# Optimization experiments

Hardware: AMD Instinct MI355X
Metric: run time of the kernel (lower is better)

Reference implementation:

```python
import jax, jax.numpy as jnp
import numpy as np

B, S, D = 2, 2048, 1024
H = 16
DH = D // H  # 64

def setup_inputs() -> dict:
    key = jax.random.key(0)
    ks = jax.random.split(key, 7)
    sc = 1.0 / np.sqrt(DH)
    return {
        "sequences": jax.random.normal(ks[0], (B, S, D), dtype=jnp.float32),
        "Wq": jax.random.normal(ks[1], (H, DH, DH), dtype=jnp.float32) * sc,
        "bq": jax.random.normal(ks[2], (H, DH), dtype=jnp.float32) * 0.02,
        "Wk": jax.random.normal(ks[3], (H, DH, DH), dtype=jnp.float32) * sc,
        "bk": jax.random.normal(ks[4], (H, DH), dtype=jnp.float32) * 0.02,
        "Wv": jax.random.normal(ks[5], (H, DH, DH), dtype=jnp.float32) * sc,
        "bv": jax.random.normal(ks[6], (H, DH), dtype=jnp.float32) * 0.02,
    }

def reference(sequences, Wq, bq, Wk, bk, Wv, bv):
    b, s, _ = sequences.shape
    x = sequences.reshape(b, s, H, DH)  # [B,S,H,Dh]
    # torch Linear: y = x @ W^T + b; W is [out,in] => einsum contracts input dim d
    q = jnp.einsum("bshd,hed->bshe", x, Wq) + bq  # [B,S,H,Dh]
    k = jnp.einsum("bshd,hed->bshe", x, Wk) + bk
    v = jnp.einsum("bshd,hed->bshe", x, Wv) + bv
    scores = jnp.einsum("bshd,bthd->bhst", q, k) / jnp.sqrt(jnp.float32(DH))
    attn = jax.nn.softmax(scores, axis=-1)  # [B,H,S,S]
    out = jnp.einsum("bhst,bthd->bshd", attn, v)  # [B,S,H,Dh]
    return out.reshape(b, s, H * DH)
```

## Files before the change

kernel.cpp:

```cpp
#include <hip/hip_runtime.h>

typedef unsigned short u16;
typedef unsigned int   u32;
typedef __bf16 bf16x8 __attribute__((ext_vector_type(8)));
typedef float  f32x4  __attribute__((ext_vector_type(4)));
typedef float  f32x16 __attribute__((ext_vector_type(16)));
typedef u16    u16x4  __attribute__((ext_vector_type(4)));
typedef u32    u32x4  __attribute__((ext_vector_type(4)));

#define HH   16
#define DHH  64
#define SEQL 2048
#define NB   2
#define BHN  (NB * HH)
#define SCLF 0.1803368801111204f

static __device__ __forceinline__ u16 f2bf(float f) {
    return __builtin_bit_cast(u16, (__bf16)f);
}
static __device__ __forceinline__ u32 pack2(float a, float b) {
    return (u32)f2bf(a) | ((u32)f2bf(b) << 16);
}
static __device__ __forceinline__ void plswap(u32 &a, u32 &b) {
    asm volatile("v_permlane32_swap_b32 %0, %1" : "+v"(a), "+v"(b));
}

static __device__ __forceinline__ void gload_lds16(const void* g, void* l) {
    __builtin_amdgcn_global_load_lds(
        (const __attribute__((address_space(1))) unsigned int*)g,
        (__attribute__((address_space(3))) unsigned int*)l, 16, 0, 0);
}

__global__ __launch_bounds__(256) void wconv_kernel(
    const float* __restrict__ Wq, const float* __restrict__ Wk,
    const float* __restrict__ Wv, u16* __restrict__ Wb)
{
    const int m = blockIdx.y;
    const float* W = (m == 0) ? Wq : (m == 1) ? Wk : Wv;
    const float s = (m == 0) ? SCLF : 1.0f;
    const int i = (blockIdx.x * 256 + threadIdx.x) * 4;
    float4 v = *reinterpret_cast<const float4*>(W + i);
    u16x4 o = { f2bf(v.x * s), f2bf(v.y * s), f2bf(v.z * s), f2bf(v.w * s) };
    *reinterpret_cast<u16x4*>(Wb + (size_t)m * 65536 + i) = o;
}

__global__ __launch_bounds__(256) void qkv_kernel(
    const float* __restrict__ x, const u16* __restrict__ Wb,
    const float* __restrict__ bq, const float* __restrict__ bk,
    const float* __restrict__ bv,
    u16* __restrict__ Qws, u16* __restrict__ Kws, u16* __restrict__ Vtws)
{
    const int h   = blockIdx.y;
    const int r0  = blockIdx.x * 64;
    const int tid = threadIdx.x;
    const int w   = tid >> 6;
    const int l   = tid & 63;
    const int c   = l & 15;
    const int g   = l >> 4;

    __shared__ u16 qt[64 * 72];
    __shared__ u16 kt[64 * 72];
    __shared__ u16 vt[64 * 72];

    bf16x8 xa[2];
    {
        const float* xp = x + (size_t)(r0 + w * 16 + c) * 1024 + h * 64 + g * 8;
        #pragma unroll
        for (int kh = 0; kh < 2; ++kh) {
            float4 lo = *reinterpret_cast<const float4*>(xp + kh * 32);
            float4 hi = *reinterpret_cast<const float4*>(xp + kh * 32 + 4);
            bf16x8 f;
            f[0]=(__bf16)lo.x; f[1]=(__bf16)lo.y; f[2]=(__bf16)lo.z; f[3]=(__bf16)lo.w;
            f[4]=(__bf16)hi.x; f[5]=(__bf16)hi.y; f[6]=(__bf16)hi.z; f[7]=(__bf16)hi.w;
            xa[kh] = f;
        }
    }

    const int b      = r0 >> 11;
    const int s_base = r0 & (SEQL - 1);
    const int bh     = b * HH + h;

    f32x4 acc[3][4];
    #pragma unroll
    for (int m = 0; m < 3; ++m)
        #pragma unroll
        for (int ct = 0; ct < 4; ++ct) {
            acc[m][ct][0] = 0.f; acc[m][ct][1] = 0.f;
            acc[m][ct][2] = 0.f; acc[m][ct][3] = 0.f;
        }
    #pragma unroll
    for (int kh = 0; kh < 2; ++kh)
        #pragma unroll
        for (int m = 0; m < 3; ++m) {
            const u16* W = Wb + (size_t)m * 65536 + h * 4096;
            #pragma unroll
            for (int ct = 0; ct < 4; ++ct) {
                bf16x8 wf = *reinterpret_cast<const bf16x8*>(
                    W + (ct * 16 + c) * 64 + kh * 32 + g * 8);
                acc[m][ct] = __builtin_amdgcn_mfma_f32_16x16x32_bf16(xa[kh], wf, acc[m][ct], 0, 0, 0);
            }
        }

    #pragma unroll
    for (int ct = 0; ct < 4; ++ct) {
        const float bbq = bq[h * 64 + ct * 16 + c] * SCLF;
        const float bbk = bk[h * 64 + ct * 16 + c];
        const float bbv = bv[h * 64 + ct * 16 + c];
        u16x4 pv;
        #pragma unroll
        for (int r = 0; r < 4; ++r) {
            const int srow = w * 16 + g * 4 + r;
            qt[srow * 72 + ct * 16 + c] = f2bf(acc[0][ct][r] + bbq);
            kt[srow * 72 + ct * 16 + c] = f2bf(acc[1][ct][r] + bbk);
            pv[r] = f2bf(acc[2][ct][r] + bbv);
        }
        *reinterpret_cast<u16x4*>(&vt[(ct * 16 + c) * 72 + w * 16 + g * 4]) = pv;
    }
    __syncthreads();

    {
        const int d  = tid >> 2;
        const int s0 = (tid & 3) * 16;
        u16* qp = Qws + ((size_t)bh * SEQL + s_base + d) * 64 + s0;
        *reinterpret_cast<uint4*>(qp)     = *reinterpret_cast<const uint4*>(&qt[d * 72 + s0]);
        *reinterpret_cast<uint4*>(qp + 8) = *reinterpret_cast<const uint4*>(&qt[d * 72 + s0 + 8]);
        u16* kp = Kws + ((size_t)bh * SEQL + s_base + d) * 64 + s0;
        *reinterpret_cast<uint4*>(kp)     = *reinterpret_cast<const uint4*>(&kt[d * 72 + s0]);
        *reinterpret_cast<uint4*>(kp + 8) = *reinterpret_cast<const uint4*>(&kt[d * 72 + s0 + 8]);
        u16* vp = Vtws + ((size_t)bh * 64 + d) * SEQL + s_base + s0;
        *reinterpret_cast<uint4*>(vp)     = *reinterpret_cast<const uint4*>(&vt[d * 72 + s0]);
        *reinterpret_cast<uint4*>(vp + 8) = *reinterpret_cast<const uint4*>(&vt[d * 72 + s0 + 8]);
    }
}

__global__ __launch_bounds__(256, 2) void attn_kernel(
    const u16* __restrict__ Qws, const u16* __restrict__ Kws,
    const u16* __restrict__ Vtws, float* __restrict__ out)
{
    const int p     = blockIdx.x;
    const int lid   = (p & 7) * 64 + (p >> 3);
    const int qtile = lid & 15;
    const int bh    = lid >> 4;
    const int b     = bh >> 4;
    const int h     = bh & 15;

    const int tid = threadIdx.x;
    const int w   = tid >> 6;
    const int l   = tid & 63;
    const int lq  = l & 31;
    const int hi  = l >> 5;
    const int q0  = qtile * 128 + w * 32;

    __shared__ u16 k_lds[2][64 * 64];
    __shared__ u16 v_lds[2][64 * 64];

    const u16* Kb = Kws  + (size_t)bh * SEQL * 64;
    const u16* Vb = Vtws + (size_t)bh * 64 * SEQL;

    const int rs8 = l >> 3;
    const int sx  = (l & 7) ^ rs8;

    #define STAGE(bb, k0)                                                     \
    {   _Pragma("unroll")                                                     \
        for (int a = 0; a < 2; ++a) {                                         \
            const int rbase = w * 16 + a * 8;                                 \
            const int r     = rbase + rs8;                                    \
            gload_lds16(Kb + (size_t)((k0) + r) * 64 + sx * 8,                \
                        &k_lds[bb][rbase * 64]);                              \
            gload_lds16(Vb + (size_t)r * SEQL + (k0) + sx * 8,                \
                        &v_lds[bb][rbase * 64]);                              \
        }                                                                     \
    }

    bf16x8 qf[4];
    #pragma unroll
    for (int s = 0; s < 4; ++s)
        qf[s] = *reinterpret_cast<const bf16x8*>(
            Qws + ((size_t)bh * SEQL + q0 + lq) * 64 + s * 16 + hi * 8);

    f32x16 zero16;
    #pragma unroll
    for (int j = 0; j < 16; ++j) zero16[j] = 0.f;

    f32x16 acc[2];
    acc[0] = zero16; acc[1] = zero16;
    float mrow = -1e30f;
    float lrow = 0.f;

    int koff[4];
    #pragma unroll
    for (int s = 0; s < 4; ++s) koff[s] = ((s * 2 + hi) ^ (lq & 7)) * 16;

    bf16x8 vfA[2][4], vfB[2][4];
    bf16x8 pfA[4], pfB[4];

    STAGE(0, 0);
    __syncthreads();

    auto body = [&](bf16x8 (&vfC)[2][4], bf16x8 (&pfC)[4],
                    bf16x8 (&vfP)[2][4], bf16x8 (&pfP)[4],
                    int t, bool has_prev) {
        const int cur = t & 1;
        if (t + 1 < SEQL / 64) STAGE(cur ^ 1, (t + 1) * 64);

        const char* kb = reinterpret_cast<const char*>(&k_lds[cur][0]);
        bf16x8 kf0[4], kf1[4];
        #pragma unroll
        for (int s = 0; s < 4; ++s) {
            kf0[s] = *reinterpret_cast<const bf16x8*>(kb + lq * 128 + koff[s]);
            kf1[s] = *reinterpret_cast<const bf16x8*>(kb + (32 + lq) * 128 + koff[s]);
        }

        __builtin_amdgcn_s_setprio(1);
        f32x16 st0 = __builtin_amdgcn_mfma_f32_32x32x16_bf16(kf0[0], qf[0], zero16, 0, 0, 0);
        f32x16 st1 = __builtin_amdgcn_mfma_f32_32x32x16_bf16(kf1[0], qf[0], zero16, 0, 0, 0);
        #pragma unroll
        for (int s = 1; s < 4; ++s) {
            st0 = __builtin_amdgcn_mfma_f32_32x32x16_bf16(kf0[s], qf[s], st0, 0, 0, 0);
            st1 = __builtin_amdgcn_mfma_f32_32x32x16_bf16(kf1[s], qf[s], st1, 0, 0, 0);
        }
        if (has_prev) {
            #pragma unroll
            for (int s = 0; s < 4; ++s) {
                acc[0] = __builtin_amdgcn_mfma_f32_32x32x16_bf16(vfP[0][s], pfP[s], acc[0], 0, 0, 0);
                acc[1] = __builtin_amdgcn_mfma_f32_32x32x16_bf16(vfP[1][s], pfP[s], acc[1], 0, 0, 0);
            }
        }
        __builtin_amdgcn_s_setprio(0);

        const char* vb = reinterpret_cast<const char*>(&v_lds[cur][0]);
        #pragma unroll
        for (int dt = 0; dt < 2; ++dt)
            #pragma unroll
            for (int s = 0; s < 4; ++s)
                vfC[dt][s] = *reinterpret_cast<const bf16x8*>(vb + (dt * 32 + lq) * 128 + koff[s]);

        float t0 = fmaxf(fmaxf(st0[0], st0[1]),  fmaxf(st0[2], st0[3]));
        float t1 = fmaxf(fmaxf(st0[4], st0[5]),  fmaxf(st0[6], st0[7]));
        float t2 = fmaxf(fmaxf(st0[8], st0[9]),  fmaxf(st0[10], st0[11]));
        float t3 = fmaxf(fmaxf(st0[12], st0[13]), fmaxf(st0[14], st0[15]));
        float t4 = fmaxf(fmaxf(st1[0], st1[1]),  fmaxf(st1[2], st1[3]));
        float t5 = fmaxf(fmaxf(st1[4], st1[5]),  fmaxf(st1[6], st1[7]));
        float t6 = fmaxf(fmaxf(st1[8], st1[9]),  fmaxf(st1[10], st1[11]));
        float t7 = fmaxf(fmaxf(st1[12], st1[13]), fmaxf(st1[14], st1[15]));
        float mx = fmaxf(fmaxf(fmaxf(t0, t1), fmaxf(t2, t3)),
                         fmaxf(fmaxf(t4, t5), fmaxf(t6, t7)));
        mx = fmaxf(mx, __shfl_xor(mx, 32, 64));

        if (!__all(mx <= mrow + 8.f)) {
            const float mn    = fmaxf(mrow, mx);
            const float alpha = __builtin_amdgcn_exp2f(mrow - mn);
            mrow = mn;
            lrow *= alpha;
            #pragma unroll
            for (int j = 0; j < 16; ++j) { acc[0][j] *= alpha; acc[1][j] *= alpha; }
        }

        float rs0 = 0.f, rs1 = 0.f;
        u32 wd[16];
        {
            float pp[16];
            #pragma unroll
            for (int r = 0; r < 16; ++r) {
                pp[r] = __builtin_amdgcn_exp2f(st0[r] - mrow);
                if (r & 1) rs1 += pp[r]; else rs0 += pp[r];
            }
            #pragma unroll
            for (int j = 0; j < 8; ++j) wd[j] = pack2(pp[2 * j], pp[2 * j + 1]);
        }
        {
            float pp[16];
            #pragma unroll
            for (int r = 0; r < 16; ++r) {
                pp[r] = __builtin_amdgcn_exp2f(st1[r] - mrow);
                if (r & 1) rs1 += pp[r]; else rs0 += pp[r];
            }
            #pragma unroll
            for (int j = 0; j < 8; ++j) wd[8 + j] = pack2(pp[2 * j], pp[2 * j + 1]);
        }
        lrow += rs0 + rs1;

        plswap(wd[0],  wd[2]);  plswap(wd[1],  wd[3]);
        plswap(wd[4],  wd[6]);  plswap(wd[5],  wd[7]);
        plswap(wd[8],  wd[10]); plswap(wd[9],  wd[11]);
        plswap(wd[12], wd[14]); plswap(wd[13], wd[15]);

        #pragma unroll
        for (int s = 0; s < 4; ++s) {
            u32x4 tmp = { wd[s * 4 + 0], wd[s * 4 + 1], wd[s * 4 + 2], wd[s * 4 + 3] };
            pfC[s] = __builtin_bit_cast(bf16x8, tmp);
        }

        __syncthreads();
    };

    for (int tt = 0; tt < SEQL / 64; tt += 2) {
        body(vfA, pfA, vfB, pfB, tt,     tt != 0);
        body(vfB, pfB, vfA, pfA, tt + 1, true);
    }

    #pragma unroll
    for (int s = 0; s < 4; ++s) {
        acc[0] = __builtin_amdgcn_mfma_f32_32x32x16_bf16(vfB[0][s], pfB[s], acc[0], 0, 0, 0);
        acc[1] = __builtin_amdgcn_mfma_f32_32x32x16_bf16(vfB[1][s], pfB[s], acc[1], 0, 0, 0);
    }
    const float inv = 1.f / (lrow + __shfl_xor(lrow, 32, 64));

    float* op = out + ((size_t)b * SEQL + q0 + lq) * 1024 + h * 64 + hi * 4;
    #pragma unroll
    for (int dt = 0; dt < 2; ++dt)
        #pragma unroll
        for (int rg = 0; rg < 4; ++rg) {
            float4 o;
            o.x = acc[dt][rg * 4 + 0] * inv;
            o.y = acc[dt][rg * 4 + 1] * inv;
            o.z = acc[dt][rg * 4 + 2] * inv;
            o.w = acc[dt][rg * 4 + 3] * inv;
            *reinterpret_cast<float4*>(op + dt * 32 + rg * 8) = o;
        }
}

extern "C" void kernel_launch(void* const* d_in, const int* in_sizes, int n_in,
                              void* d_out, int out_size, void* d_ws, size_t ws_size,
                              hipStream_t stream) {
    const float* x  = (const float*)d_in[0];
    const float* Wq = (const float*)d_in[1];
    const float* bq = (const float*)d_in[2];
    const float* Wk = (const float*)d_in[3];
    const float* bk = (const float*)d_in[4];
    const float* Wv = (const float*)d_in[5];
    const float* bv = (const float*)d_in[6];
    float* out = (float*)d_out;

    const size_t per = (size_t)BHN * SEQL * 64;
    u16* Qws = (u16*)d_ws;
    u16* Kws = Qws + per;
    u16* Vt  = Kws + per;
    u16* Wb  = Vt  + per;

    wconv_kernel<<<dim3(64, 3), 256, 0, stream>>>(Wq, Wk, Wv, Wb);
    qkv_kernel<<<dim3(64, 16), 256, 0, stream>>>(x, Wb, bq, bk, bv, Qws, Kws, Vt);
    attn_kernel<<<dim3(512), 256, 0, stream>>>(Qws, Kws, Vt, out);
}
```

Measured before the change: 84.96 us.

## Split KV sequence across two wave groups per block and merge softmax partials

Doubles waves per block, with two groups each handling alternating KV tiles, halving each wave's serial loop and raising occupancy. Partial accumulators, maxima and sums from one group are written to reused LDS and merged by the other with log-sum-exp rescaling. The launch bound of 512 threads with 4 blocks per CU tightens the register budget, which risks spills, and LDS use per block doubles.

```diff
diff --git a/kernel.cpp b/kernel.cpp
--- a/kernel.cpp
+++ b/kernel.cpp
@@ -14,6 +14,7 @@
 #define NB   2
 #define BHN  (NB * HH)
 #define SCLF 0.1803368801111204f
+#define NI   16
 
 static __device__ __forceinline__ u16 f2bf(float f) {
     return __builtin_bit_cast(u16, (__bf16)f);
@@ -133,7 +134,7 @@
     }
 }
 
-__global__ __launch_bounds__(256, 2) void attn_kernel(
+__global__ __launch_bounds__(512, 4) void attn_kernel(
     const u16* __restrict__ Qws, const u16* __restrict__ Kws,
     const u16* __restrict__ Vtws, float* __restrict__ out)
 {
@@ -146,13 +147,15 @@
 
     const int tid = threadIdx.x;
     const int w   = tid >> 6;
+    const int wl  = w & 3;
+    const int grp = w >> 2;
     const int l   = tid & 63;
     const int lq  = l & 31;
     const int hi  = l >> 5;
-    const int q0  = qtile * 128 + w * 32;
-
-    __shared__ u16 k_lds[2][64 * 64];
-    __shared__ u16 v_lds[2][64 * 64];
+    const int q0  = qtile * 128 + wl * 32;
+
+    __shared__ u16 k_lds[2][2][64 * 64];
+    __shared__ u16 v_lds[2][2][64 * 64];
 
     const u16* Kb = Kws  + (size_t)bh * SEQL * 64;
     const u16* Vb = Vtws + (size_t)bh * 64 * SEQL;
@@ -163,12 +166,12 @@
     #define STAGE(bb, k0)                                                     \
     {   _Pragma("unroll")                                                     \
         for (int a = 0; a < 2; ++a) {                                         \
-            const int rbase = w * 16 + a * 8;                                 \
+            const int rbase = wl * 16 + a * 8;                                \
             const int r     = rbase + rs8;                                    \
             gload_lds16(Kb + (size_t)((k0) + r) * 64 + sx * 8,                \
-                        &k_lds[bb][rbase * 64]);                              \
+                        &k_lds[bb][grp][rbase * 64]);                         \
             gload_lds16(Vb + (size_t)r * SEQL + (k0) + sx * 8,                \
-                        &v_lds[bb][rbase * 64]);                              \
+                        &v_lds[bb][grp][rbase * 64]);                         \
         }                                                                     \
     }
 
@@ -194,16 +197,16 @@
     bf16x8 vfA[2][4], vfB[2][4];
     bf16x8 pfA[4], pfB[4];
 
-    STAGE(0, 0);
+    STAGE(0, grp * 64);
     __syncthreads();
 
     auto body = [&](bf16x8 (&vfC)[2][4], bf16x8 (&pfC)[4],
                     bf16x8 (&vfP)[2][4], bf16x8 (&pfP)[4],
-                    int t, bool has_prev) {
-        const int cur = t & 1;
-        if (t + 1 < SEQL / 64) STAGE(cur ^ 1, (t + 1) * 64);
-
-        const char* kb = reinterpret_cast<const char*>(&k_lds[cur][0]);
+                    int i, bool has_prev) {
+        const int cur = i & 1;
+        if (i + 1 < NI) STAGE(cur ^ 1, (2 * (i + 1) + grp) * 64);
+
+        const char* kb = reinterpret_cast<const char*>(&k_lds[cur][grp][0]);
         bf16x8 kf0[4], kf1[4];
         #pragma unroll
         for (int s = 0; s < 4; ++s) {
@@ -228,7 +231,7 @@
         }
         __builtin_amdgcn_s_setprio(0);
 
-        const char* vb = reinterpret_cast<const char*>(&v_lds[cur][0]);
+        const char* vb = reinterpret_cast<const char*>(&v_lds[cur][grp][0]);
         #pragma unroll
         for (int dt = 0; dt < 2; ++dt)
             #pragma unroll
@@ -294,9 +297,9 @@
         __syncthreads();
     };
 
-    for (int tt = 0; tt < SEQL / 64; tt += 2) {
-        body(vfA, pfA, vfB, pfB, tt,     tt != 0);
-        body(vfB, pfB, vfA, pfA, tt + 1, true);
+    for (int ii = 0; ii < NI; ii += 2) {
+        body(vfA, pfA, vfB, pfB, ii,     ii != 0);
+        body(vfB, pfB, vfA, pfA, ii + 1, true);
     }
 
     #pragma unroll
@@ -304,20 +307,38 @@
         acc[0] = __builtin_amdgcn_mfma_f32_32x32x16_bf16(vfB[0][s], pfB[s], acc[0], 0, 0, 0);
         acc[1] = __builtin_amdgcn_mfma_f32_32x32x16_bf16(vfB[1][s], pfB[s], acc[1], 0, 0, 0);
     }
-    const float inv = 1.f / (lrow + __shfl_xor(lrow, 32, 64));
-
-    float* op = out + ((size_t)b * SEQL + q0 + lq) * 1024 + h * 64 + hi * 4;
-    #pragma unroll
-    for (int dt = 0; dt < 2; ++dt)
-        #pragma unroll
-        for (int rg = 0; rg < 4; ++rg) {
-            float4 o;
-            o.x = acc[dt][rg * 4 + 0] * inv;
-            o.y = acc[dt][rg * 4 + 1] * inv;
-            o.z = acc[dt][rg * 4 + 2] * inv;
-            o.w = acc[dt][rg * 4 + 3] * inv;
-            *reinterpret_cast<float4*>(op + dt * 32 + rg * 8) = o;
-        }
+    const float lt = lrow + __shfl_xor(lrow, 32, 64);
+
+    float* mbase = (wl < 2) ? reinterpret_cast<float*>(&k_lds[0][0][0])
+                            : reinterpret_cast<float*>(&v_lds[0][0][0]);
+    float* mb = mbase + (size_t)(wl & 1) * (64 * 36) + l * 36;
+
+    if (grp == 1) {
+        #pragma unroll
+        for (int j = 0; j < 16; ++j) { mb[j] = acc[0][j]; mb[16 + j] = acc[1][j]; }
+        mb[32] = mrow; mb[33] = lt;
+    }
+    __syncthreads();
+    if (grp == 0) {
+        const float mB = mb[32], lB = mb[33];
+        const float mn = fmaxf(mrow, mB);
+        const float aA = __builtin_amdgcn_exp2f(mrow - mn);
+        const float aB = __builtin_amdgcn_exp2f(mB - mn);
+        const float inv = 1.f / (lt * aA + lB * aB);
+
+        float* op = out + ((size_t)b * SEQL + q0 + lq) * 1024 + h * 64 + hi * 4;
+        #pragma unroll
+        for (int dt = 0; dt < 2; ++dt)
+            #pragma unroll
+            for (int rg = 0; rg < 4; ++rg) {
+                float4 o;
+                #pragma unroll
+                for (int j = 0; j < 4; ++j)
+                    ((float*)&o)[j] = (acc[dt][rg * 4 + j] * aA +
+                                       mb[dt * 16 + rg * 4 + j] * aB) * inv;
+                *reinterpret_cast<float4*>(op + dt * 32 + rg * 8) = o;
+            }
+    }
 }
 
 extern "C" void kernel_launch(void* const* d_in, const int* in_sizes, int n_in,
@@ -340,5 +361,5 @@
 
     wconv_kernel<<<dim3(64, 3), 256, 0, stream>>>(Wq, Wk, Wv, Wb);
     qkv_kernel<<<dim3(64, 16), 256, 0, stream>>>(x, Wb, bq, bk, bv, Qws, Kws, Vt);
-    attn_kernel<<<dim3(512), 256, 0, stream>>>(Qws, Kws, Vt, out);
-}
+    attn_kernel<<<dim3(512), 512, 0, stream>>>(Qws, Kws, Vt, out);
+}
```

New measurement: 241.5 us. 184% more time.
